# Optimization experiments

Measured on AMD Instinct MI355X. Metric: run time of the kernel, lower is better.

## Reference

```python
import jax, jax.numpy as jnp
import numpy as np

N_NODES = 100000


def _gcn_norm(edge_index, n):
    # add self-loops, then symmetric deg^{-1/2} normalization (PyG GCNConv default)
    loop = jnp.arange(n, dtype=edge_index.dtype)
    src = jnp.concatenate([edge_index[0], loop])
    dst = jnp.concatenate([edge_index[1], loop])
    ones = jnp.ones(src.shape[0], dtype=jnp.float32)
    deg = jax.ops.segment_sum(ones, dst, num_segments=n)
    dinv = jnp.where(deg > 0, jax.lax.rsqrt(deg), 0.0)
    norm = dinv[src] * dinv[dst]  # [E + N]
    return src, dst, norm


def _gcn_conv(x, src, dst, norm, W, b, n):
    h = x @ W                                    # [N, out] transform first (out <= in)
    msg = norm[:, None] * h[src]                 # [E+N, out]
    agg = jax.ops.segment_sum(msg, dst, num_segments=n)
    return agg + b


def reference(x, edge_index, W1, b1, W2, b2):
    n = x.shape[0]
    src, dst, norm = _gcn_norm(edge_index, n)
    h = jax.nn.relu(_gcn_conv(x, src, dst, norm, W1, b1, n))
    # dropout is identity in eval mode (training=False)
    h = jax.nn.relu(_gcn_conv(h, src, dst, norm, W2, b2, n))
    return jax.nn.log_softmax(h, axis=1)


def setup_inputs() -> dict:
    key = jax.random.key(0)
    k1, k2, k3, k4 = jax.random.split(key, 4)
    n, e, f, h, c = N_NODES, 1600000, 500, 64, 40
    x = jax.random.normal(k1, (n, f), dtype=jnp.float32)
    edge_index = jax.random.randint(k2, (2, e), 0, n, dtype=jnp.int64)
    W1 = jax.random.normal(k3, (f, h), dtype=jnp.float32) * (1.0 / np.sqrt(f))
    b1 = jnp.zeros((h,), dtype=jnp.float32)
    W2 = jax.random.normal(k4, (h, c), dtype=jnp.float32) * (1.0 / np.sqrt(h))
    b2 = jnp.zeros((c,), dtype=jnp.float32)
    return {"x": x, "edge_index": edge_index, "W1": W1, "b1": b1, "W2": W2, "b2": b2}
```

## Files before the change

kernel.cpp:

```cpp
#include <hip/hip_runtime.h>

#define NN_F 500
#define HID 64
#define NC 40
#define SCAN_T 256
#define SCAN_E 8
#define SCAN_B (SCAN_T * SCAN_E)
#define LDS_S 40

typedef short s8v __attribute__((ext_vector_type(8)));
typedef short s4v __attribute__((ext_vector_type(4)));
typedef float f4v __attribute__((ext_vector_type(4)));

__device__ __forceinline__ unsigned short rne_bf16(float x) {
    unsigned u = __float_as_uint(x);
    return (unsigned short)((u + 0x7fffu + ((u >> 16) & 1u)) >> 16);
}
__device__ __forceinline__ float bf16_lo(unsigned v) {
    return __uint_as_float(v << 16);
}
__device__ __forceinline__ float bf16_hi(unsigned v) {
    return __uint_as_float(v & 0xffff0000u);
}

__device__ __forceinline__ int load_edge(const void* ei, long long idx, int is64) {
    if (is64) return (int)((const long long*)ei)[idx];
    return ((const int*)ei)[idx];
}

__global__ __launch_bounds__(256) void detect_kernel(const unsigned int* w, int* flag) {
    __shared__ unsigned int red[256];
    unsigned int acc = 0;
    for (int i = threadIdx.x; i < 2048; i += 256) acc |= w[2 * i + 1];
    red[threadIdx.x] = acc;
    __syncthreads();
    for (int s = 128; s > 0; s >>= 1) {
        if (threadIdx.x < s) red[threadIdx.x] |= red[threadIdx.x + s];
        __syncthreads();
    }
    if (threadIdx.x == 0) flag[0] = (red[0] == 0u) ? 1 : 0;
}

__global__ __launch_bounds__(256) void deg_kernel(const void* ei, const int* flag,
                                                  int* deg, int E) {
    int is64 = flag[0];
    long long e = (long long)blockIdx.x * 256 + threadIdx.x;
    if (e < E) {
        int d = load_edge(ei, (long long)E + e, is64);
        atomicAdd(&deg[d], 1);
    }
}

__global__ __launch_bounds__(SCAN_T) void scan1(const int* __restrict__ deg,
                                                int* __restrict__ off,
                                                int* __restrict__ bsums,
                                                float* __restrict__ dinv, int n) {
    __shared__ int lds[SCAN_T];
    int base = blockIdx.x * SCAN_B + threadIdx.x * SCAN_E;
    int v[SCAN_E];
    int local = 0;
#pragma unroll
    for (int k = 0; k < SCAN_E; ++k) {
        int i = base + k;
        v[k] = (i < n) ? deg[i] : 0;
        if (i < n) dinv[i] = rsqrtf((float)v[k] + 1.0f);
        local += v[k];
    }
    lds[threadIdx.x] = local;
    __syncthreads();
    for (int o = 1; o < SCAN_T; o <<= 1) {
        int t = (threadIdx.x >= o) ? lds[threadIdx.x - o] : 0;
        __syncthreads();
        lds[threadIdx.x] += t;
        __syncthreads();
    }
    int prefix = lds[threadIdx.x] - local;
    if (threadIdx.x == SCAN_T - 1) bsums[blockIdx.x] = lds[threadIdx.x];
    int run = prefix;
#pragma unroll
    for (int k = 0; k < SCAN_E; ++k) {
        if (base + k < n) { off[base + k] = run; run += v[k]; }
    }
}

__global__ void scan2(int* bsums, int* off, int nb, int n) {
    int lane = threadIdx.x;
    if (nb <= 64) {
        int v = (lane < nb) ? bsums[lane] : 0;
        int incl = v;
#pragma unroll
        for (int o = 1; o < 64; o <<= 1) {
            int t = __shfl_up(incl, o);
            if (lane >= o) incl += t;
        }
        if (lane < nb) bsums[lane] = incl - v;
        if (lane == 63) off[n] = incl;
    } else if (lane == 0) {
        int run = 0;
        for (int i = 0; i < nb; ++i) { int t = bsums[i]; bsums[i] = run; run += t; }
        off[n] = run;
    }
}

__global__ __launch_bounds__(SCAN_T) void scan3(int* __restrict__ off,
                                                int* __restrict__ cur,
                                                const int* __restrict__ bsums, int n) {
    int base = blockIdx.x * SCAN_B + threadIdx.x * SCAN_E;
    int add = bsums[blockIdx.x];
#pragma unroll
    for (int k = 0; k < SCAN_E; ++k) {
        int i = base + k;
        if (i < n) { int v = off[i] + add; off[i] = v; cur[i] = v; }
    }
}

__global__ __launch_bounds__(256) void build_kernel(const void* ei, const int* flag,
                                                    const float* __restrict__ dinv,
                                                    int* __restrict__ cur,
                                                    int2* __restrict__ csr, int E) {
    int is64 = flag[0];
    long long e = (long long)blockIdx.x * 256 + threadIdx.x;
    if (e >= E) return;
    int s = load_edge(ei, e, is64);
    int d = load_edge(ei, (long long)E + e, is64);
    int pos = atomicAdd(&cur[d], 1);
    csr[pos] = make_int2(s, (int)__float_as_uint(dinv[s] * dinv[d]));
}

__global__ __launch_bounds__(256) void wprep2(const float* __restrict__ W1,
                                              const float* __restrict__ W2,
                                              unsigned short* __restrict__ Wt1,
                                              unsigned short* __restrict__ Wt2) {
    int id = blockIdx.x * 256 + threadIdx.x;
    if (id < 64 * 512) {
        int nn = id >> 9, k = id & 511;
        float v = (k < NN_F) ? W1[k * HID + nn] : 0.f;
        Wt1[id] = rne_bf16(v);
    } else {
        int id2 = id - 64 * 512;
        if (id2 >= 64 * 64) return;
        int nn = id2 >> 6, k = id2 & 63;
        float v = (nn < NC) ? W2[k * NC + nn] : 0.f;
        Wt2[id2] = rne_bf16(v);
    }
}

template<int KPAD>
__global__ __launch_bounds__(256) void gemm_mfma(const float* __restrict__ A,
                                                 const unsigned short* __restrict__ Wh,
                                                 unsigned short* __restrict__ out,
                                                 int n, int K) {
    __shared__ unsigned short Xh[128 * LDS_S];
    __shared__ unsigned short Bh[64 * LDS_S];
    const int t = threadIdx.x;
    const int row0 = blockIdx.x * 128;
    const int wid = t >> 6, lane = t & 63, q = lane >> 4, nn = lane & 15;

    f4v acc[2][4];
#pragma unroll
    for (int mt = 0; mt < 2; ++mt)
#pragma unroll
        for (int ct = 0; ct < 4; ++ct) acc[mt][ct] = (f4v){0.f, 0.f, 0.f, 0.f};

    for (int k0 = 0; k0 < KPAD; k0 += 32) {
        {
            int bn = t >> 2, kq = t & 3;
            *(s8v*)&Bh[bn * LDS_S + kq * 8] = *(const s8v*)&Wh[bn * KPAD + k0 + kq * 8];
        }
        {
            int kq = t & 7, rbase = t >> 3;
#pragma unroll
            for (int rr = 0; rr < 4; ++rr) {
                int row = rr * 32 + rbase;
                int grow = row0 + row;
                int k = k0 + kq * 4;
                float v0 = 0.f, v1 = 0.f, v2 = 0.f, v3 = 0.f;
                if (grow < n) {
                    if (k + 4 <= K) {
                        float4 v = *(const float4*)&A[(long long)grow * K + k];
                        v0 = v.x; v1 = v.y; v2 = v.z; v3 = v.w;
                    } else {
                        if (k + 0 < K) v0 = A[(long long)grow * K + k + 0];
                        if (k + 1 < K) v1 = A[(long long)grow * K + k + 1];
                        if (k + 2 < K) v2 = A[(long long)grow * K + k + 2];
                        if (k + 3 < K) v3 = A[(long long)grow * K + k + 3];
                    }
                }
                s4v h4;
                h4[0] = (short)rne_bf16(v0);
                h4[1] = (short)rne_bf16(v1);
                h4[2] = (short)rne_bf16(v2);
                h4[3] = (short)rne_bf16(v3);
                *(s4v*)&Xh[row * LDS_S + kq * 4] = h4;
            }
        }
        __syncthreads();

        const s8v ah0 = *(const s8v*)&Xh[(wid * 32 + nn) * LDS_S + q * 8];
        const s8v ah1 = *(const s8v*)&Xh[(wid * 32 + 16 + nn) * LDS_S + q * 8];
#pragma unroll
        for (int ct = 0; ct < 4; ++ct) {
            const s8v bh = *(const s8v*)&Bh[(ct * 16 + nn) * LDS_S + q * 8];
            acc[0][ct] = __builtin_amdgcn_mfma_f32_16x16x32_bf16(ah0, bh, acc[0][ct], 0, 0, 0);
            acc[1][ct] = __builtin_amdgcn_mfma_f32_16x16x32_bf16(ah1, bh, acc[1][ct], 0, 0, 0);
        }
        __syncthreads();
    }

#pragma unroll
    for (int mt = 0; mt < 2; ++mt)
#pragma unroll
        for (int ct = 0; ct < 4; ++ct)
#pragma unroll
            for (int r = 0; r < 4; ++r) {
                int row = row0 + wid * 32 + mt * 16 + q * 4 + r;
                if (row < n) out[(long long)row * 64 + ct * 16 + nn] = rne_bf16(acc[mt][ct][r]);
            }
}

__global__ __launch_bounds__(256) void gather_l1(const int2* __restrict__ csr,
                                                 const int* __restrict__ off,
                                                 const unsigned short* __restrict__ h,
                                                 const float* __restrict__ dinv,
                                                 const float* __restrict__ b,
                                                 float* __restrict__ agg, int n) {
    const int lane = threadIdx.x & 63;
    const int g = lane >> 4, fp = lane & 15;
    const int node = __builtin_amdgcn_readfirstlane(blockIdx.x * 4 + (threadIdx.x >> 6));
    if (node >= n) return;
    const int start = off[node], end = off[node + 1];
    f4v acc = (f4v){0.f, 0.f, 0.f, 0.f};
    int j = start;
    for (; j + 8 <= end; j += 8) {
        int2 ea = csr[j + g];
        int2 eb = csr[j + 4 + g];
        uint2 ha = *(const uint2*)(h + (long long)ea.x * 64 + fp * 4);
        uint2 hb = *(const uint2*)(h + (long long)eb.x * 64 + fp * 4);
        float wa = __uint_as_float((unsigned)ea.y);
        float wb = __uint_as_float((unsigned)eb.y);
        acc[0] = fmaf(wa, bf16_lo(ha.x), acc[0]);
        acc[1] = fmaf(wa, bf16_hi(ha.x), acc[1]);
        acc[2] = fmaf(wa, bf16_lo(ha.y), acc[2]);
        acc[3] = fmaf(wa, bf16_hi(ha.y), acc[3]);
        acc[0] = fmaf(wb, bf16_lo(hb.x), acc[0]);
        acc[1] = fmaf(wb, bf16_hi(hb.x), acc[1]);
        acc[2] = fmaf(wb, bf16_lo(hb.y), acc[2]);
        acc[3] = fmaf(wb, bf16_hi(hb.y), acc[3]);
    }
    for (; j < end; j += 4) {
        int jj = j + g;
        int2 e = csr[jj < end ? jj : end - 1];
        float w = (jj < end) ? __uint_as_float((unsigned)e.y) : 0.f;
        uint2 hv = *(const uint2*)(h + (long long)e.x * 64 + fp * 4);
        acc[0] = fmaf(w, bf16_lo(hv.x), acc[0]);
        acc[1] = fmaf(w, bf16_hi(hv.x), acc[1]);
        acc[2] = fmaf(w, bf16_lo(hv.y), acc[2]);
        acc[3] = fmaf(w, bf16_hi(hv.y), acc[3]);
    }
#pragma unroll
    for (int k = 0; k < 4; ++k) {
        acc[k] += __shfl_xor(acc[k], 16);
        acc[k] += __shfl_xor(acc[k], 32);
    }
    float dv = dinv[node];
    uint2 hn = *(const uint2*)(h + (long long)node * 64 + fp * 4);
    acc[0] = fmaf(dv * dv, bf16_lo(hn.x), acc[0]);
    acc[1] = fmaf(dv * dv, bf16_hi(hn.x), acc[1]);
    acc[2] = fmaf(dv * dv, bf16_lo(hn.y), acc[2]);
    acc[3] = fmaf(dv * dv, bf16_hi(hn.y), acc[3]);
    float4 b4 = ((const float4*)b)[fp];
    if (g == 0) {
        float4 v;
        v.x = acc[0] + b4.x; v.x = v.x > 0.f ? v.x : 0.f;
        v.y = acc[1] + b4.y; v.y = v.y > 0.f ? v.y : 0.f;
        v.z = acc[2] + b4.z; v.z = v.z > 0.f ? v.z : 0.f;
        v.w = acc[3] + b4.w; v.w = v.w > 0.f ? v.w : 0.f;
        ((float4*)(agg + (long long)node * 64))[fp] = v;
    }
}

__global__ __launch_bounds__(256) void gather_l2(const int2* __restrict__ csr,
                                                 const int* __restrict__ off,
                                                 const unsigned short* __restrict__ h,
                                                 const float* __restrict__ dinv,
                                                 const float* __restrict__ b,
                                                 float* __restrict__ out, int n) {
    const int lane = threadIdx.x & 63;
    const int g = lane >> 4, fp = lane & 15;
    const int node = __builtin_amdgcn_readfirstlane(blockIdx.x * 4 + (threadIdx.x >> 6));
    if (node >= n) return;
    const int start = off[node], end = off[node + 1];
    f4v acc = (f4v){0.f, 0.f, 0.f, 0.f};
    int j = start;
    for (; j + 8 <= end; j += 8) {
        int2 ea = csr[j + g];
        int2 eb = csr[j + 4 + g];
        uint2 ha = *(const uint2*)(h + (long long)ea.x * 64 + fp * 4);
        uint2 hb = *(const uint2*)(h + (long long)eb.x * 64 + fp * 4);
        float wa = __uint_as_float((unsigned)ea.y);
        float wb = __uint_as_float((unsigned)eb.y);
        acc[0] = fmaf(wa, bf16_lo(ha.x), acc[0]);
        acc[1] = fmaf(wa, bf16_hi(ha.x), acc[1]);
        acc[2] = fmaf(wa, bf16_lo(ha.y), acc[2]);
        acc[3] = fmaf(wa, bf16_hi(ha.y), acc[3]);
        acc[0] = fmaf(wb, bf16_lo(hb.x), acc[0]);
        acc[1] = fmaf(wb, bf16_hi(hb.x), acc[1]);
        acc[2] = fmaf(wb, bf16_lo(hb.y), acc[2]);
        acc[3] = fmaf(wb, bf16_hi(hb.y), acc[3]);
    }
    for (; j < end; j += 4) {
        int jj = j + g;
        int2 e = csr[jj < end ? jj : end - 1];
        float w = (jj < end) ? __uint_as_float((unsigned)e.y) : 0.f;
        uint2 hv = *(const uint2*)(h + (long long)e.x * 64 + fp * 4);
        acc[0] = fmaf(w, bf16_lo(hv.x), acc[0]);
        acc[1] = fmaf(w, bf16_hi(hv.x), acc[1]);
        acc[2] = fmaf(w, bf16_lo(hv.y), acc[2]);
        acc[3] = fmaf(w, bf16_hi(hv.y), acc[3]);
    }
#pragma unroll
    for (int k = 0; k < 4; ++k) {
        acc[k] += __shfl_xor(acc[k], 16);
        acc[k] += __shfl_xor(acc[k], 32);
    }
    float dv = dinv[node];
    uint2 hn = *(const uint2*)(h + (long long)node * 64 + fp * 4);
    acc[0] = fmaf(dv * dv, bf16_lo(hn.x), acc[0]);
    acc[1] = fmaf(dv * dv, bf16_hi(hn.x), acc[1]);
    acc[2] = fmaf(dv * dv, bf16_lo(hn.y), acc[2]);
    acc[3] = fmaf(dv * dv, bf16_hi(hn.y), acc[3]);
    float t0, t1, t2, t3;
    if (fp < 10) {
        float4 b4 = ((const float4*)b)[fp];
        t0 = acc[0] + b4.x; t0 = t0 > 0.f ? t0 : 0.f;
        t1 = acc[1] + b4.y; t1 = t1 > 0.f ? t1 : 0.f;
        t2 = acc[2] + b4.z; t2 = t2 > 0.f ? t2 : 0.f;
        t3 = acc[3] + b4.w; t3 = t3 > 0.f ? t3 : 0.f;
    } else {
        t0 = t1 = t2 = t3 = -1e30f;
    }
    float m = fmaxf(fmaxf(t0, t1), fmaxf(t2, t3));
#pragma unroll
    for (int o = 1; o < 16; o <<= 1) m = fmaxf(m, __shfl_xor(m, o));
    float ssum = 0.f;
    if (fp < 10) ssum = expf(t0 - m) + expf(t1 - m) + expf(t2 - m) + expf(t3 - m);
#pragma unroll
    for (int o = 1; o < 16; o <<= 1) ssum += __shfl_xor(ssum, o);
    if (g == 0 && fp < 10) {
        float ls = m + logf(ssum);
        float4 v = make_float4(t0 - ls, t1 - ls, t2 - ls, t3 - ls);
        ((float4*)(out + (long long)node * NC))[fp] = v;
    }
}

static inline char* align256(char* p) {
    return (char*)(((uintptr_t)p + 255) & ~(uintptr_t)255);
}

extern "C" void kernel_launch(void* const* d_in, const int* in_sizes, int n_in,
                              void* d_out, int out_size, void* d_ws, size_t ws_size,
                              hipStream_t stream) {
    const float* x  = (const float*)d_in[0];
    const void*  ei = d_in[1];
    const float* W1 = (const float*)d_in[2];
    const float* b1 = (const float*)d_in[3];
    const float* W2 = (const float*)d_in[4];
    const float* b2 = (const float*)d_in[5];
    float* out = (float*)d_out;
    const int n = in_sizes[0] / NN_F;
    const int E = in_sizes[1] / 2;
    const int nScanBlocks = (n + SCAN_B - 1) / SCAN_B;

    char* p = (char*)d_ws;
    int* flag = (int*)p;                 p = align256(p + 16 * sizeof(int));
    int* deg  = (int*)p;                 p = align256(p + (size_t)n * sizeof(int));
    int* off  = (int*)p;                 p = align256(p + (size_t)(n + 1) * sizeof(int));
    int* cur  = (int*)p;                 p = align256(p + (size_t)n * sizeof(int));
    int* bsums = (int*)p;                p = align256(p + 256 * sizeof(int));
    float* dinv = (float*)p;             p = align256(p + (size_t)n * sizeof(float));
    int2* csr = (int2*)p;                p = align256(p + (size_t)E * sizeof(int2));
    unsigned short* Wt1 = (unsigned short*)p; p = align256(p + (size_t)64 * 512 * sizeof(short));
    unsigned short* Wt2 = (unsigned short*)p; p = align256(p + (size_t)64 * 64 * sizeof(short));
    unsigned short* h1 = (unsigned short*)p; p = align256(p + (size_t)n * 64 * sizeof(unsigned short));
    float* agg1 = (float*)p;             p = align256(p + (size_t)n * 64 * sizeof(float));
    unsigned short* h2 = h1;

    (void)hipMemsetAsync(deg, 0, (size_t)n * sizeof(int), stream);
    detect_kernel<<<1, 256, 0, stream>>>((const unsigned int*)ei, flag);
    deg_kernel<<<(E + 255) / 256, 256, 0, stream>>>(ei, flag, deg, E);

    scan1<<<nScanBlocks, SCAN_T, 0, stream>>>(deg, off, bsums, dinv, n);
    scan2<<<1, 64, 0, stream>>>(bsums, off, nScanBlocks, n);
    scan3<<<nScanBlocks, SCAN_T, 0, stream>>>(off, cur, bsums, n);
    build_kernel<<<(E + 255) / 256, 256, 0, stream>>>(ei, flag, dinv, cur, csr, E);

    wprep2<<<(64 * 512 + 64 * 64 + 255) / 256, 256, 0, stream>>>(W1, W2, Wt1, Wt2);

    const int gBlocks = (n + 127) / 128;
    gemm_mfma<512><<<gBlocks, 256, 0, stream>>>(x, Wt1, h1, n, NN_F);
    gather_l1<<<(n + 3) / 4, 256, 0, stream>>>(csr, off, h1, dinv, b1, agg1, n);

    gemm_mfma<64><<<gBlocks, 256, 0, stream>>>(agg1, Wt2, h2, n, HID);
    gather_l2<<<(n + 3) / 4, 256, 0, stream>>>(csr, off, h2, dinv, b2, out, n);
}
```

Before: 586.9 us.

## Fuse W2 transform into layer-1 gather, merge prep kernels, shrink GEMM tile

Result: slower. 645.7 us (+10.0%).

```diff
diff --git a/kernel.cpp b/kernel.cpp
--- a/kernel.cpp
+++ b/kernel.cpp
@@ -28,22 +28,31 @@
     return ((const int*)ei)[idx];
 }
 
-__global__ __launch_bounds__(256) void detect_kernel(const unsigned int* w, int* flag) {
-    __shared__ unsigned int red[256];
+__device__ __forceinline__ int detect_is64_block(const void* ei, int E) {
+    const unsigned int* w = (const unsigned int*)ei;
     unsigned int acc = 0;
-    for (int i = threadIdx.x; i < 2048; i += 256) acc |= w[2 * i + 1];
-    red[threadIdx.x] = acc;
+    int i = threadIdx.x;
+    if (i < 256 && i < E) acc = w[2 * i + 1];
+    int any = __any(acc != 0u);
+    __shared__ int red[4];
+    if ((threadIdx.x & 63) == 0) red[threadIdx.x >> 6] = any;
     __syncthreads();
-    for (int s = 128; s > 0; s >>= 1) {
-        if (threadIdx.x < s) red[threadIdx.x] |= red[threadIdx.x + s];
-        __syncthreads();
-    }
-    if (threadIdx.x == 0) flag[0] = (red[0] == 0u) ? 1 : 0;
-}
-
-__global__ __launch_bounds__(256) void deg_kernel(const void* ei, const int* flag,
-                                                  int* deg, int E) {
-    int is64 = flag[0];
+    return (red[0] | red[1] | red[2] | red[3]) == 0;
+}
+
+__global__ __launch_bounds__(256) void deg_wprep(const void* ei, int* __restrict__ deg,
+                                                 const float* __restrict__ W1,
+                                                 unsigned short* __restrict__ Wt1,
+                                                 int E, int degBlocks) {
+    if ((int)blockIdx.x >= degBlocks) {
+        int id = ((int)blockIdx.x - degBlocks) * 256 + threadIdx.x;
+        if (id < 64 * 512) {
+            int nn = id >> 9, k = id & 511;
+            Wt1[id] = rne_bf16(k < NN_F ? W1[k * HID + nn] : 0.f);
+        }
+        return;
+    }
+    int is64 = detect_is64_block(ei, E);
     long long e = (long long)blockIdx.x * 256 + threadIdx.x;
     if (e < E) {
         int d = load_edge(ei, (long long)E + e, is64);
@@ -83,25 +92,31 @@
     }
 }
 
+__global__ __launch_bounds__(SCAN_T) void scan_fin(int* __restrict__ off,
+                                                   int* __restrict__ cur,
+                                                   const int* __restrict__ bsums,
+                                                   int n, int nb) {
+    const int lane = threadIdx.x & 63;
+    int v = (lane < nb && lane < (int)blockIdx.x) ? bsums[lane] : 0;
+#pragma unroll
+    for (int o = 1; o < 64; o <<= 1) v += __shfl_xor(v, o);
+    const int add = v;
+    if ((int)blockIdx.x == nb - 1 && threadIdx.x == 0) off[n] = add + bsums[nb - 1];
+    int base = blockIdx.x * SCAN_B + threadIdx.x * SCAN_E;
+#pragma unroll
+    for (int k = 0; k < SCAN_E; ++k) {
+        int i = base + k;
+        if (i < n) { int t = off[i] + add; off[i] = t; cur[i] = t; }
+    }
+}
+
 __global__ void scan2(int* bsums, int* off, int nb, int n) {
-    int lane = threadIdx.x;
-    if (nb <= 64) {
-        int v = (lane < nb) ? bsums[lane] : 0;
-        int incl = v;
-#pragma unroll
-        for (int o = 1; o < 64; o <<= 1) {
-            int t = __shfl_up(incl, o);
-            if (lane >= o) incl += t;
-        }
-        if (lane < nb) bsums[lane] = incl - v;
-        if (lane == 63) off[n] = incl;
-    } else if (lane == 0) {
+    if (threadIdx.x == 0 && blockIdx.x == 0) {
         int run = 0;
         for (int i = 0; i < nb; ++i) { int t = bsums[i]; bsums[i] = run; run += t; }
         off[n] = run;
     }
 }
-
 __global__ __launch_bounds__(SCAN_T) void scan3(int* __restrict__ off,
                                                 int* __restrict__ cur,
                                                 const int* __restrict__ bsums, int n) {
@@ -114,11 +129,11 @@
     }
 }
 
-__global__ __launch_bounds__(256) void build_kernel(const void* ei, const int* flag,
+__global__ __launch_bounds__(256) void build_kernel(const void* ei,
                                                     const float* __restrict__ dinv,
                                                     int* __restrict__ cur,
                                                     int2* __restrict__ csr, int E) {
-    int is64 = flag[0];
+    int is64 = detect_is64_block(ei, E);
     long long e = (long long)blockIdx.x * 256 + threadIdx.x;
     if (e >= E) return;
     int s = load_edge(ei, e, is64);
@@ -127,50 +142,29 @@
     csr[pos] = make_int2(s, (int)__float_as_uint(dinv[s] * dinv[d]));
 }
 
-__global__ __launch_bounds__(256) void wprep2(const float* __restrict__ W1,
-                                              const float* __restrict__ W2,
-                                              unsigned short* __restrict__ Wt1,
-                                              unsigned short* __restrict__ Wt2) {
-    int id = blockIdx.x * 256 + threadIdx.x;
-    if (id < 64 * 512) {
-        int nn = id >> 9, k = id & 511;
-        float v = (k < NN_F) ? W1[k * HID + nn] : 0.f;
-        Wt1[id] = rne_bf16(v);
-    } else {
-        int id2 = id - 64 * 512;
-        if (id2 >= 64 * 64) return;
-        int nn = id2 >> 6, k = id2 & 63;
-        float v = (nn < NC) ? W2[k * NC + nn] : 0.f;
-        Wt2[id2] = rne_bf16(v);
-    }
-}
-
-template<int KPAD>
 __global__ __launch_bounds__(256) void gemm_mfma(const float* __restrict__ A,
                                                  const unsigned short* __restrict__ Wh,
                                                  unsigned short* __restrict__ out,
                                                  int n, int K) {
-    __shared__ unsigned short Xh[128 * LDS_S];
+    __shared__ unsigned short Xh[64 * LDS_S];
     __shared__ unsigned short Bh[64 * LDS_S];
     const int t = threadIdx.x;
-    const int row0 = blockIdx.x * 128;
+    const int row0 = blockIdx.x * 64;
     const int wid = t >> 6, lane = t & 63, q = lane >> 4, nn = lane & 15;
 
-    f4v acc[2][4];
-#pragma unroll
-    for (int mt = 0; mt < 2; ++mt)
-#pragma unroll
-        for (int ct = 0; ct < 4; ++ct) acc[mt][ct] = (f4v){0.f, 0.f, 0.f, 0.f};
-
-    for (int k0 = 0; k0 < KPAD; k0 += 32) {
+    f4v acc[4];
+#pragma unroll
+    for (int ct = 0; ct < 4; ++ct) acc[ct] = (f4v){0.f, 0.f, 0.f, 0.f};
+
+    for (int k0 = 0; k0 < 512; k0 += 32) {
         {
             int bn = t >> 2, kq = t & 3;
-            *(s8v*)&Bh[bn * LDS_S + kq * 8] = *(const s8v*)&Wh[bn * KPAD + k0 + kq * 8];
+            *(s8v*)&Bh[bn * LDS_S + kq * 8] = *(const s8v*)&Wh[bn * 512 + k0 + kq * 8];
         }
         {
             int kq = t & 7, rbase = t >> 3;
 #pragma unroll
-            for (int rr = 0; rr < 4; ++rr) {
+            for (int rr = 0; rr < 2; ++rr) {
                 int row = rr * 32 + rbase;
                 int grow = row0 + row;
                 int k = k0 + kq * 4;
@@ -196,34 +190,35 @@
         }
         __syncthreads();
 
-        const s8v ah0 = *(const s8v*)&Xh[(wid * 32 + nn) * LDS_S + q * 8];
-        const s8v ah1 = *(const s8v*)&Xh[(wid * 32 + 16 + nn) * LDS_S + q * 8];
+        const s8v ah = *(const s8v*)&Xh[(wid * 16 + nn) * LDS_S + q * 8];
 #pragma unroll
         for (int ct = 0; ct < 4; ++ct) {
             const s8v bh = *(const s8v*)&Bh[(ct * 16 + nn) * LDS_S + q * 8];
-            acc[0][ct] = __builtin_amdgcn_mfma_f32_16x16x32_bf16(ah0, bh, acc[0][ct], 0, 0, 0);
-            acc[1][ct] = __builtin_amdgcn_mfma_f32_16x16x32_bf16(ah1, bh, acc[1][ct], 0, 0, 0);
+            acc[ct] = __builtin_amdgcn_mfma_f32_16x16x32_bf16(ah, bh, acc[ct], 0, 0, 0);
         }
         __syncthreads();
     }
 
 #pragma unroll
-    for (int mt = 0; mt < 2; ++mt)
-#pragma unroll
-        for (int ct = 0; ct < 4; ++ct)
-#pragma unroll
-            for (int r = 0; r < 4; ++r) {
-                int row = row0 + wid * 32 + mt * 16 + q * 4 + r;
-                if (row < n) out[(long long)row * 64 + ct * 16 + nn] = rne_bf16(acc[mt][ct][r]);
-            }
-}
-
-__global__ __launch_bounds__(256) void gather_l1(const int2* __restrict__ csr,
-                                                 const int* __restrict__ off,
-                                                 const unsigned short* __restrict__ h,
-                                                 const float* __restrict__ dinv,
-                                                 const float* __restrict__ b,
-                                                 float* __restrict__ agg, int n) {
+    for (int ct = 0; ct < 4; ++ct)
+#pragma unroll
+        for (int r = 0; r < 4; ++r) {
+            int row = row0 + wid * 16 + q * 4 + r;
+            if (row < n) out[(long long)row * 64 + ct * 16 + nn] = rne_bf16(acc[ct][r]);
+        }
+}
+
+__global__ __launch_bounds__(256) void gather_l1w2(const int2* __restrict__ csr,
+                                                   const int* __restrict__ off,
+                                                   const unsigned short* __restrict__ h,
+                                                   const float* __restrict__ dinv,
+                                                   const float* __restrict__ b,
+                                                   const float* __restrict__ W2,
+                                                   unsigned short* __restrict__ h2, int n) {
+    __shared__ float W2s[HID * NC];
+    for (int i = threadIdx.x; i < HID * NC; i += 256) W2s[i] = W2[i];
+    __syncthreads();
+
     const int lane = threadIdx.x & 63;
     const int g = lane >> 4, fp = lane & 15;
     const int node = __builtin_amdgcn_readfirstlane(blockIdx.x * 4 + (threadIdx.x >> 6));
@@ -269,14 +264,26 @@
     acc[2] = fmaf(dv * dv, bf16_lo(hn.y), acc[2]);
     acc[3] = fmaf(dv * dv, bf16_hi(hn.y), acc[3]);
     float4 b4 = ((const float4*)b)[fp];
-    if (g == 0) {
-        float4 v;
-        v.x = acc[0] + b4.x; v.x = v.x > 0.f ? v.x : 0.f;
-        v.y = acc[1] + b4.y; v.y = v.y > 0.f ? v.y : 0.f;
-        v.z = acc[2] + b4.z; v.z = v.z > 0.f ? v.z : 0.f;
-        v.w = acc[3] + b4.w; v.w = v.w > 0.f ? v.w : 0.f;
-        ((float4*)(agg + (long long)node * 64))[fp] = v;
-    }
+    float v0 = acc[0] + b4.x; v0 = v0 > 0.f ? v0 : 0.f;
+    float v1 = acc[1] + b4.y; v1 = v1 > 0.f ? v1 : 0.f;
+    float v2 = acc[2] + b4.z; v2 = v2 > 0.f ? v2 : 0.f;
+    float v3 = acc[3] + b4.w; v3 = v3 > 0.f ? v3 : 0.f;
+
+    float hcol = 0.f;
+#pragma unroll
+    for (int fp0 = 0; fp0 < 16; ++fp0) {
+        float a0 = __shfl(v0, fp0);
+        float a1 = __shfl(v1, fp0);
+        float a2 = __shfl(v2, fp0);
+        float a3 = __shfl(v3, fp0);
+        if (lane < NC) {
+            hcol = fmaf(a0, W2s[(4 * fp0 + 0) * NC + lane], hcol);
+            hcol = fmaf(a1, W2s[(4 * fp0 + 1) * NC + lane], hcol);
+            hcol = fmaf(a2, W2s[(4 * fp0 + 2) * NC + lane], hcol);
+            hcol = fmaf(a3, W2s[(4 * fp0 + 3) * NC + lane], hcol);
+        }
+    }
+    h2[(long long)node * 64 + lane] = rne_bf16(hcol);
 }
 
 __global__ __launch_bounds__(256) void gather_l2(const int2* __restrict__ csr,
@@ -295,28 +302,32 @@
     for (; j + 8 <= end; j += 8) {
         int2 ea = csr[j + g];
         int2 eb = csr[j + 4 + g];
-        uint2 ha = *(const uint2*)(h + (long long)ea.x * 64 + fp * 4);
-        uint2 hb = *(const uint2*)(h + (long long)eb.x * 64 + fp * 4);
-        float wa = __uint_as_float((unsigned)ea.y);
-        float wb = __uint_as_float((unsigned)eb.y);
-        acc[0] = fmaf(wa, bf16_lo(ha.x), acc[0]);
-        acc[1] = fmaf(wa, bf16_hi(ha.x), acc[1]);
-        acc[2] = fmaf(wa, bf16_lo(ha.y), acc[2]);
-        acc[3] = fmaf(wa, bf16_hi(ha.y), acc[3]);
-        acc[0] = fmaf(wb, bf16_lo(hb.x), acc[0]);
-        acc[1] = fmaf(wb, bf16_hi(hb.x), acc[1]);
-        acc[2] = fmaf(wb, bf16_lo(hb.y), acc[2]);
-        acc[3] = fmaf(wb, bf16_hi(hb.y), acc[3]);
+        if (fp < 10) {
+            uint2 ha = *(const uint2*)(h + (long long)ea.x * 64 + fp * 4);
+            uint2 hb = *(const uint2*)(h + (long long)eb.x * 64 + fp * 4);
+            float wa = __uint_as_float((unsigned)ea.y);
+            float wb = __uint_as_float((unsigned)eb.y);
+            acc[0] = fmaf(wa, bf16_lo(ha.x), acc[0]);
+            acc[1] = fmaf(wa, bf16_hi(ha.x), acc[1]);
+            acc[2] = fmaf(wa, bf16_lo(ha.y), acc[2]);
+            acc[3] = fmaf(wa, bf16_hi(ha.y), acc[3]);
+            acc[0] = fmaf(wb, bf16_lo(hb.x), acc[0]);
+            acc[1] = fmaf(wb, bf16_hi(hb.x), acc[1]);
+            acc[2] = fmaf(wb, bf16_lo(hb.y), acc[2]);
+            acc[3] = fmaf(wb, bf16_hi(hb.y), acc[3]);
+        }
     }
     for (; j < end; j += 4) {
         int jj = j + g;
         int2 e = csr[jj < end ? jj : end - 1];
-        float w = (jj < end) ? __uint_as_float((unsigned)e.y) : 0.f;
-        uint2 hv = *(const uint2*)(h + (long long)e.x * 64 + fp * 4);
-        acc[0] = fmaf(w, bf16_lo(hv.x), acc[0]);
-        acc[1] = fmaf(w, bf16_hi(hv.x), acc[1]);
-        acc[2] = fmaf(w, bf16_lo(hv.y), acc[2]);
-        acc[3] = fmaf(w, bf16_hi(hv.y), acc[3]);
+        if (fp < 10) {
+            float w = (jj < end) ? __uint_as_float((unsigned)e.y) : 0.f;
+            uint2 hv = *(const uint2*)(h + (long long)e.x * 64 + fp * 4);
+            acc[0] = fmaf(w, bf16_lo(hv.x), acc[0]);
+            acc[1] = fmaf(w, bf16_hi(hv.x), acc[1]);
+            acc[2] = fmaf(w, bf16_lo(hv.y), acc[2]);
+            acc[3] = fmaf(w, bf16_hi(hv.y), acc[3]);
+        }
     }
 #pragma unroll
     for (int k = 0; k < 4; ++k) {
@@ -324,11 +335,13 @@
         acc[k] += __shfl_xor(acc[k], 32);
     }
     float dv = dinv[node];
-    uint2 hn = *(const uint2*)(h + (long long)node * 64 + fp * 4);
-    acc[0] = fmaf(dv * dv, bf16_lo(hn.x), acc[0]);
-    acc[1] = fmaf(dv * dv, bf16_hi(hn.x), acc[1]);
-    acc[2] = fmaf(dv * dv, bf16_lo(hn.y), acc[2]);
-    acc[3] = fmaf(dv * dv, bf16_hi(hn.y), acc[3]);
+    if (fp < 10) {
+        uint2 hn = *(const uint2*)(h + (long long)node * 64 + fp * 4);
+        acc[0] = fmaf(dv * dv, bf16_lo(hn.x), acc[0]);
+        acc[1] = fmaf(dv * dv, bf16_hi(hn.x), acc[1]);
+        acc[2] = fmaf(dv * dv, bf16_lo(hn.y), acc[2]);
+        acc[3] = fmaf(dv * dv, bf16_hi(hn.y), acc[3]);
+    }
     float t0, t1, t2, t3;
     if (fp < 10) {
         float4 b4 = ((const float4*)b)[fp];
@@ -370,9 +383,9 @@
     const int n = in_sizes[0] / NN_F;
     const int E = in_sizes[1] / 2;
     const int nScanBlocks = (n + SCAN_B - 1) / SCAN_B;
+    const int degBlocks = (E + 255) / 256;
 
     char* p = (char*)d_ws;
-    int* flag = (int*)p;                 p = align256(p + 16 * sizeof(int));
     int* deg  = (int*)p;                 p = align256(p + (size_t)n * sizeof(int));
     int* off  = (int*)p;                 p = align256(p + (size_t)(n + 1) * sizeof(int));
     int* cur  = (int*)p;                 p = align256(p + (size_t)n * sizeof(int));
@@ -380,26 +393,22 @@
     float* dinv = (float*)p;             p = align256(p + (size_t)n * sizeof(float));
     int2* csr = (int2*)p;                p = align256(p + (size_t)E * sizeof(int2));
     unsigned short* Wt1 = (unsigned short*)p; p = align256(p + (size_t)64 * 512 * sizeof(short));
-    unsigned short* Wt2 = (unsigned short*)p; p = align256(p + (size_t)64 * 64 * sizeof(short));
     unsigned short* h1 = (unsigned short*)p; p = align256(p + (size_t)n * 64 * sizeof(unsigned short));
-    float* agg1 = (float*)p;             p = align256(p + (size_t)n * 64 * sizeof(float));
-    unsigned short* h2 = h1;
+    unsigned short* h2 = (unsigned short*)p; p = align256(p + (size_t)n * 64 * sizeof(unsigned short));
 
     (void)hipMemsetAsync(deg, 0, (size_t)n * sizeof(int), stream);
-    detect_kernel<<<1, 256, 0, stream>>>((const unsigned int*)ei, flag);
-    deg_kernel<<<(E + 255) / 256, 256, 0, stream>>>(ei, flag, deg, E);
+    deg_wprep<<<degBlocks + 128, 256, 0, stream>>>(ei, deg, W1, Wt1, E, degBlocks);
 
     scan1<<<nScanBlocks, SCAN_T, 0, stream>>>(deg, off, bsums, dinv, n);
-    scan2<<<1, 64, 0, stream>>>(bsums, off, nScanBlocks, n);
-    scan3<<<nScanBlocks, SCAN_T, 0, stream>>>(off, cur, bsums, n);
-    build_kernel<<<(E + 255) / 256, 256, 0, stream>>>(ei, flag, dinv, cur, csr, E);
-
-    wprep2<<<(64 * 512 + 64 * 64 + 255) / 256, 256, 0, stream>>>(W1, W2, Wt1, Wt2);
-
-    const int gBlocks = (n + 127) / 128;
-    gemm_mfma<512><<<gBlocks, 256, 0, stream>>>(x, Wt1, h1, n, NN_F);
-    gather_l1<<<(n + 3) / 4, 256, 0, stream>>>(csr, off, h1, dinv, b1, agg1, n);
-
-    gemm_mfma<64><<<gBlocks, 256, 0, stream>>>(agg1, Wt2, h2, n, HID);
+    if (nScanBlocks <= 64) {
+        scan_fin<<<nScanBlocks, SCAN_T, 0, stream>>>(off, cur, bsums, n, nScanBlocks);
+    } else {
+        scan2<<<1, 64, 0, stream>>>(bsums, off, nScanBlocks, n);
+        scan3<<<nScanBlocks, SCAN_T, 0, stream>>>(off, cur, bsums, n);
+    }
+    build_kernel<<<degBlocks, 256, 0, stream>>>(ei, dinv, cur, csr, E);
+
+    gemm_mfma<<<(n + 63) / 64, 256, 0, stream>>>(x, Wt1, h1, n, NN_F);
+    gather_l1w2<<<(n + 3) / 4, 256, 0, stream>>>(csr, off, h1, dinv, b1, W2, h2, n);
     gather_l2<<<(n + 3) / 4, 256, 0, stream>>>(csr, off, h2, dinv, b2, out, n);
 }
```
